# Kernel tuning notes

Hardware: AMD Instinct MI355X
Metric: run time of the kernel (lower is better)

## Reference

```python
import jax, jax.numpy as jnp
import numpy as np

D, NH, DH, DHR, DC = 2048, 16, 128, 64, 1024
B, L = 2, 2048
EPS = 1e-6


def _rms(x, w):
    return x * jax.lax.rsqrt(jnp.mean(x * x, axis=-1, keepdims=True) + EPS) * w


def _rope_tables(seq_len, dim, dtype):
    inv_freq = 1.0 / (10000.0 ** (jnp.arange(0, dim, 2, dtype=jnp.float32) / dim))
    freqs = jnp.arange(seq_len, dtype=jnp.float32)[:, None] * inv_freq[None, :]  # [L, dim/2]
    emb = jnp.concatenate([freqs, freqs], axis=-1)                               # [L, dim]
    return jnp.cos(emb).astype(dtype), jnp.sin(emb).astype(dtype)


def _apply_rope(x, cos, sin):
    # x: [B, H, L, dhr]
    half = x.shape[-1] // 2
    x1, x2 = x[..., :half], x[..., half:]
    rot = jnp.concatenate([-x2, x1], axis=-1)
    return x * cos[None, None] + rot * sin[None, None]


def setup_inputs() -> dict:
    key = jax.random.key(0)
    ks = jax.random.split(key, 14)
    s = 0.02
    inp = {
        "x": jax.random.normal(ks[0], (B, L, D), dtype=jnp.float32),
        "W_DKV": jax.random.normal(ks[1], (D, DC), dtype=jnp.float32) * s,
        "kv_norm_w": 1.0 + 0.01 * jax.random.normal(ks[2], (DC,), dtype=jnp.float32),
        "W_UK": jax.random.normal(ks[3], (DC, NH * DH), dtype=jnp.float32) * s,
        "W_UV": jax.random.normal(ks[4], (DC, NH * DH), dtype=jnp.float32) * s,
        "W_DQ": jax.random.normal(ks[5], (D, DC), dtype=jnp.float32) * s,
        "q_norm_w": 1.0 + 0.01 * jax.random.normal(ks[6], (DC,), dtype=jnp.float32),
        "W_UQ": jax.random.normal(ks[7], (DC, 2 * NH * DH), dtype=jnp.float32) * s,
        "W_QR": jax.random.normal(ks[8], (DC, 2 * NH * DHR), dtype=jnp.float32) * s,
        "W_KR": jax.random.normal(ks[9], (D, DHR), dtype=jnp.float32) * s,
        "W_lambda_w": jax.random.normal(ks[10], (D, NH), dtype=jnp.float32) * s,
        "W_lambda_b": jax.random.normal(ks[11], (NH,), dtype=jnp.float32) * s,
        "W_out": jax.random.normal(ks[12], (D, D), dtype=jnp.float32) * s,
    }
    return inp


def reference(x, W_DKV, kv_norm_w, W_UK, W_UV, W_DQ, q_norm_w, W_UQ, W_QR,
              W_KR, W_lambda_w, W_lambda_b, W_out):
    Bx, Lx, Dx = x.shape
    nh, dh, dhr = NH, DH, DHR
    dq = dh + dhr  # per-head query/key dim after decoupled-RoPE concat (192)
    scale = 1.0 / jnp.sqrt(jnp.asarray(dq, dtype=x.dtype))

    # MLA KV path
    c_kv = _rms(x @ W_DKV, kv_norm_w)                                   # [B,L,dc]
    k_c = (c_kv @ W_UK).reshape(Bx, Lx, nh, dh).transpose(0, 2, 1, 3)    # [B,nh,L,dh]
    v = (c_kv @ W_UV).reshape(Bx, Lx, nh, dh).transpose(0, 2, 1, 3)      # [B,nh,L,dh]

    # MLA Q path (doubled heads for Diff V2)
    c_q = _rms(x @ W_DQ, q_norm_w)                                       # [B,L,dcq]
    q_c = (c_q @ W_UQ).reshape(Bx, Lx, 2 * nh, dh).transpose(0, 2, 1, 3)  # [B,2nh,L,dh]

    # Decoupled RoPE
    cos, sin = _rope_tables(Lx, dhr, x.dtype)
    q_r = _apply_rope((c_q @ W_QR).reshape(Bx, Lx, 2 * nh, dhr).transpose(0, 2, 1, 3), cos, sin)
    k_r = _apply_rope((x @ W_KR).reshape(Bx, Lx, 1, dhr).transpose(0, 2, 1, 3), cos, sin)  # [B,1,L,dhr]

    q = jnp.concatenate([q_c, q_r], axis=-1)                             # [B,2nh,L,dq]
    k = jnp.concatenate([k_c, jnp.broadcast_to(k_r, (Bx, nh, Lx, dhr))], axis=-1)  # [B,nh,L,dq]

    # repeat_interleave(2) on K/V == pairing two consecutive Q heads with one K/V head
    qp = q.reshape(Bx, nh, 2, Lx, dq)                                    # [B,nh,2,L,dq]
    scores = jnp.einsum('bnpld,bnmd->bnplm', qp, k) * scale              # [B,nh,2,L,L]
    causal = jnp.tril(jnp.ones((Lx, Lx), dtype=bool))
    scores = jnp.where(causal[None, None, None], scores, jnp.finfo(scores.dtype).min)
    p = jax.nn.softmax(scores, axis=-1)
    attn = jnp.einsum('bnplm,bnmd->bnpld', p, v)                         # [B,nh,2,L,dh]

    attn1, attn2 = attn[:, :, 0], attn[:, :, 1]                          # [B,nh,L,dh]
    lam = jax.nn.sigmoid(x @ W_lambda_w + W_lambda_b)                    # [B,L,nh]
    lam = lam.transpose(0, 2, 1)[..., None]                              # [B,nh,L,1]
    out = (attn1 - lam * attn2).transpose(0, 2, 1, 3).reshape(Bx, Lx, Dx)
    return out @ W_out
```

## Files before the change

kernel.cpp:

```cpp
#include <hip/hip_runtime.h>
#include <cstddef>
#include <cstdint>


namespace {

constexpr int kDC = 1024, kDim = 2048;
constexpr float kScale = 0.07216878364870323f;
constexpr int kTA = 2128;

typedef __bf16 bf16x8 __attribute__((ext_vector_type(8)));
typedef float f32x4 __attribute__((ext_vector_type(4)));

__device__ __forceinline__ unsigned short f2bf(float f) {
  __bf16 h = (__bf16)f;
  return __builtin_bit_cast(unsigned short, h);
}
__device__ __forceinline__ float bf2f(unsigned short h) {
  union { unsigned int u; float f; } v; v.u = ((unsigned int)h) << 16;
  return v.f;
}
__device__ __forceinline__ f32x4 mfma16(bf16x8 a, bf16x8 b, f32x4 c) {
  return __builtin_amdgcn_mfma_f32_16x16x32_bf16(a, b, c, 0, 0, 0);
}
__device__ __forceinline__ void gl_lds16(const void* g, void* l) {
  __builtin_amdgcn_global_load_lds(
      (const __attribute__((address_space(1))) unsigned int*)g,
      (__attribute__((address_space(3))) unsigned int*)l, 16, 0, 0);
}
__device__ __forceinline__ void wait_lgkm0() {
  asm volatile("s_waitcnt lgkmcnt(0)" ::: "memory");
}

__global__ __launch_bounds__(256) void conv_bf16_kernel(const float* __restrict__ in,
                                                        unsigned short* __restrict__ out, int n4) {
  int e = blockIdx.x * 256 + threadIdx.x;
  if (e >= n4) return;
  float4 v = reinterpret_cast<const float4*>(in)[e];
  uint2 pk;
  pk.x = (unsigned int)f2bf(v.x) | ((unsigned int)f2bf(v.y) << 16);
  pk.y = (unsigned int)f2bf(v.z) | ((unsigned int)f2bf(v.w) << 16);
  reinterpret_cast<uint2*>(out)[e] = pk;
}

__global__ __launch_bounds__(256) void zero_bf16_kernel(unsigned short* __restrict__ out, int n8) {
  int e = blockIdx.x * 256 + threadIdx.x;
  if (e >= n8) return;
  reinterpret_cast<uint4*>(out)[e] = uint4{0, 0, 0, 0};
}

__global__ __launch_bounds__(256) void transpose_conv_kernel(const float* __restrict__ in,
                                                             unsigned short* __restrict__ out,
                                                             int K, int N) {
  __shared__ float t[32][33];
  int n0 = blockIdx.x * 32, k0 = blockIdx.y * 32;
  int tx = threadIdx.x & 31, ty = threadIdx.x >> 5;
#pragma unroll
  for (int i = 0; i < 4; i++) t[ty + i * 8][tx] = in[(size_t)(k0 + ty + i * 8) * N + n0 + tx];
  __syncthreads();
#pragma unroll
  for (int i = 0; i < 4; i++)
    out[(size_t)(n0 + ty + i * 8) * K + k0 + tx] = f2bf(t[tx][ty + i * 8]);
}

__global__ __launch_bounds__(256) void lamw_transpose_kernel(const float* __restrict__ in,
                                                             unsigned short* __restrict__ out) {
  int e = blockIdx.x * 256 + threadIdx.x;
  if (e >= 16 * 2048) return;
  int k = e & 2047, n = e >> 11;
  out[(size_t)(2112 + n) * 2048 + k] = f2bf(in[(size_t)k * 16 + n]);
}

template <int MODE>
__device__ __forceinline__ void epi_store(void* dst, void* dst2, int gr, int gc, int N, float v) {
  if (MODE == 0) {
    reinterpret_cast<float*>(dst)[(size_t)gr * N + gc] = v;
  } else if (MODE == 4) {
    if (gc < kTA) reinterpret_cast<float*>(dst)[(size_t)gr * kTA + gc] = v;
  } else if (MODE == 5) {
    int bb = gr >> 11, l = gr & 2047;
    unsigned short hv = f2bf(v);
    if (gc < 2048) {
      int h = gc >> 7, d2 = gc & 127;
      int d2s = d2 ^ ((l & 7) << 3);
      reinterpret_cast<unsigned short*>(dst)[((size_t)((bb * 16 + h) * 2048 + l)) * 192 + d2s] = hv;
    } else {
      int g2 = gc - 2048, h = g2 >> 7, d2 = g2 & 127;
      reinterpret_cast<unsigned short*>(dst2)[((size_t)((bb * 16 + h) * 128 + d2)) * 2048 + l] = hv;
    }
  } else if (MODE == 6) {
    int bb = gr >> 11, l = gr & 2047;
    if (gc < 4096) {
      int h2 = gc >> 7, d2 = gc & 127;
      reinterpret_cast<unsigned short*>(dst)[((size_t)((bb * 32 + h2) * 2048 + l)) * 192 + d2] =
          f2bf(v * kScale);
    } else {
      reinterpret_cast<unsigned short*>(dst2)[(size_t)gr * 2048 + (gc - 4096)] = f2bf(v);
    }
  }
}

template <int MODE>
__global__ __launch_bounds__(256) void gemm128_kernel(const unsigned short* __restrict__ A,
                                                      const unsigned short* __restrict__ Bt,
                                                      void* __restrict__ dst, void* __restrict__ dst2,
                                                      int M, int N, int K) {
  __shared__ unsigned short lds_a[128 * 32];
  __shared__ unsigned short lds_b[128 * 32];
  int tid = threadIdx.x, lane = tid & 63, w = tid >> 6;
  int quad = lane >> 4, l16 = lane & 15;
  int wr = w >> 1, wc = w & 1;
  int nwg = gridDim.x * gridDim.y;
  int bid = blockIdx.y * gridDim.x + blockIdx.x;
  int cpx = nwg >> 3;
  int swz = (bid & 7) * cpx + (bid >> 3);
  int bx = swz % gridDim.x, by = swz / gridDim.x;
  int mbase = by * 128, nbase = bx * 128;
  f32x4 acc[4][4] = {};
  int srow0 = tid >> 2, skoff = (tid & 3) * 8;
  const size_t a_base = (size_t)(mbase + srow0) * K + skoff;
  const size_t b_base = (size_t)(nbase + srow0) * K + skoff;
  unsigned short* lba0 = &lds_a[(size_t)(w * 64) * 8];
  unsigned short* lba1 = &lds_a[(size_t)(256 + w * 64) * 8];
  unsigned short* lbb0 = &lds_b[(size_t)(w * 64) * 8];
  unsigned short* lbb1 = &lds_b[(size_t)(256 + w * 64) * 8];
  for (int k0 = 0; k0 < K; k0 += 32) {
    __syncthreads();
    gl_lds16(&A[a_base + k0], lba0);
    gl_lds16(&A[a_base + (size_t)64 * K + k0], lba1);
    gl_lds16(&Bt[b_base + k0], lbb0);
    gl_lds16(&Bt[b_base + (size_t)64 * K + k0], lbb1);
    __syncthreads();
    bf16x8 af[4], bfr[4];
#pragma unroll
    for (int i = 0; i < 4; i++) {
      af[i] = *reinterpret_cast<const bf16x8*>(&lds_a[(wr * 64 + i * 16 + l16) * 32 + quad * 8]);
      bfr[i] = *reinterpret_cast<const bf16x8*>(&lds_b[(wc * 64 + i * 16 + l16) * 32 + quad * 8]);
    }
#pragma unroll
    for (int i = 0; i < 4; i++)
#pragma unroll
      for (int j = 0; j < 4; j++) acc[i][j] = mfma16(af[i], bfr[j], acc[i][j]);
  }
#pragma unroll
  for (int i = 0; i < 4; i++)
#pragma unroll
    for (int j = 0; j < 4; j++)
#pragma unroll
      for (int r = 0; r < 4; r++) {
        int gr = mbase + wr * 64 + i * 16 + quad * 4 + r;
        int gc = nbase + wc * 64 + j * 16 + l16;
        epi_store<MODE>(dst, dst2, gr, gc, N, acc[i][j][r]);
      }
}

__global__ __launch_bounds__(256) void rms_kernel(const float* __restrict__ in,
                                                  const float* __restrict__ w,
                                                  unsigned short* __restrict__ out, int colOff) {
  int row = blockIdx.x, tid = threadIdx.x;
  float4 v = reinterpret_cast<const float4*>(in + (size_t)row * kTA + colOff)[tid];
  float ss = v.x * v.x + v.y * v.y + v.z * v.z + v.w * v.w;
  ss += __shfl_xor(ss, 1); ss += __shfl_xor(ss, 2); ss += __shfl_xor(ss, 4);
  ss += __shfl_xor(ss, 8); ss += __shfl_xor(ss, 16); ss += __shfl_xor(ss, 32);
  __shared__ float red[4];
  if ((tid & 63) == 0) red[tid >> 6] = ss;
  __syncthreads();
  float tot = red[0] + red[1] + red[2] + red[3];
  float rs = rsqrtf(tot * (1.0f / kDC) + 1e-6f);
  float4 wv = reinterpret_cast<const float4*>(w)[tid];
  uint2 pk;
  pk.x = (unsigned int)f2bf(v.x * rs * wv.x) | ((unsigned int)f2bf(v.y * rs * wv.y) << 16);
  pk.y = (unsigned int)f2bf(v.z * rs * wv.z) | ((unsigned int)f2bf(v.w * rs * wv.w) << 16);
  reinterpret_cast<uint2*>(out)[(size_t)row * 256 + tid] = pk;
}

__device__ __forceinline__ float rope_val(float x1, float x2, int j, int l) {
  int i = j & 31;
  float inv_freq = powf(10000.0f, -(float)i * (1.0f / 32.0f));
  float ang = (float)l * inv_freq;
  float cv = cosf(ang), sv = sinf(ang);
  float rot = (j < 32) ? -x2 : x2;
  return x1 * cv + rot * sv;
}

__global__ __launch_bounds__(256) void rope_q_kernel(const unsigned short* __restrict__ qr_raw,
                                                     unsigned short* __restrict__ q_all) {
  size_t e = (size_t)blockIdx.x * 256 + threadIdx.x;
  int j = (int)(e & 63);
  int h2 = (int)((e >> 6) & 31);
  int bl = (int)(e >> 11);
  int l = bl & 2047, b = bl >> 11;
  float x1 = bf2f(qr_raw[(size_t)bl * 2048 + h2 * 64 + j]);
  float x2 = bf2f(qr_raw[(size_t)bl * 2048 + h2 * 64 + (j ^ 32)]);
  float val = rope_val(x1, x2, j, l) * kScale;
  q_all[((size_t)((b * 32 + h2) * 2048 + l)) * 192 + 128 + j] = f2bf(val);
}

__global__ __launch_bounds__(256) void rope_k_kernel(const float* __restrict__ tmpAll,
                                                     unsigned short* __restrict__ k_all) {
  size_t e = (size_t)blockIdx.x * 256 + threadIdx.x;
  int j = (int)(e & 63);
  int bl = (int)(e >> 6);
  int l = bl & 2047, b = bl >> 11;
  float x1 = tmpAll[(size_t)bl * kTA + 2048 + j];
  float x2 = tmpAll[(size_t)bl * kTA + 2048 + (j ^ 32)];
  unsigned short hv = f2bf(rope_val(x1, x2, j, l));
  int js = j ^ ((l & 7) << 3);
#pragma unroll
  for (int h = 0; h < 16; h++)
    k_all[((size_t)((b * 16 + h) * 2048 + l)) * 192 + 128 + js] = hv;
}

__global__ __launch_bounds__(256) void lam_fin_kernel(const float* __restrict__ tmpAll,
                                                      const float* __restrict__ bl_,
                                                      float* __restrict__ lam) {
  int e = blockIdx.x * 256 + threadIdx.x;
  if (e >= 4096 * 16) return;
  int n = e & 15, row = e >> 4;
  float z = tmpAll[(size_t)row * kTA + 2112 + n] + bl_[n];
  lam[e] = 1.f / (1.f + __expf(-z));
}

__global__ __launch_bounds__(256, 2) void attn7_kernel(const unsigned short* __restrict__ q_all,
                                                       const unsigned short* __restrict__ k_all,
                                                       const unsigned short* __restrict__ v_allT,
                                                       unsigned short* __restrict__ attn_o) {
  __shared__ unsigned short lds_k[2][32 * 192];
  __shared__ unsigned short lds_p[8 * 640];
  int n = blockIdx.x, qp = blockIdx.y, b = blockIdx.z;
  int tid = threadIdx.x, lane = tid & 63, w = tid >> 6, quad = lane >> 4, l16 = lane & 15;
  const unsigned short* k_head = k_all + ((size_t)(b * 16 + n) * 2048) * 192;
  const unsigned short* v_head = v_allT + ((size_t)(b * 16 + n) * 128) * 2048;

  unsigned short* pw0 = &lds_p[(w * 2 + 0) * 640];
  unsigned short* pw1 = &lds_p[(w * 2 + 1) * 640];
  const unsigned short* v_lane = v_head + (size_t)l16 * 2048 + quad * 8;

  __bf16 onec = __builtin_bit_cast(__bf16, (unsigned short)(l16 == 0 ? 0x3F80 : 0));
  bf16x8 vone = {onec, onec, onec, onec, onec, onec, onec, onec};

  auto stageK = [&](int pos0, int buf) {
    const unsigned short* kg = k_head + (size_t)pos0 * 192 + w * 1536 + lane * 8;
    unsigned short* kl = &lds_k[buf][w * 1536];
    gl_lds16(kg, kl);
    gl_lds16(kg + 512, kl + 512);
    gl_lds16(kg + 1024, kl + 1024);
  };

#pragma unroll 1
  for (int phase = 0; phase < 2; ++phase) {
    int qt = phase ? qp : (31 - qp);
    const unsigned short* q0_row =
        q_all + ((size_t)(b * 32 + 2 * n) * 2048 + qt * 64 + w * 16 + l16) * 192;
    const unsigned short* q1_row = q0_row + (size_t)2048 * 192;

    bf16x8 qf0[6], qf1[6];
#pragma unroll
    for (int ks = 0; ks < 6; ks++) {
      qf0[ks] = *reinterpret_cast<const bf16x8*>(&q0_row[ks * 32 + quad * 8]);
      qf1[ks] = *reinterpret_cast<const bf16x8*>(&q1_row[ks * 32 + quad * 8]);
    }

    f32x4 acc0[9] = {}, acc1[9] = {};
    int qlo = qt * 64 + w * 16;
    int nt = 2 * qt + 2;

    stageK(0, 0);
    for (int kt = 0; kt < nt; kt++) {
      int cur = kt & 1;
      int pos0 = kt * 32;
      __syncthreads();
      bool active = (pos0 <= qlo + 15);
      bf16x8 vf[8];
      if (active) {
        const unsigned short* vg = v_lane + pos0;
#pragma unroll
        for (int dt = 0; dt < 8; dt++)
          vf[dt] = *reinterpret_cast<const bf16x8*>(&vg[(size_t)dt * 16 * 2048]);
      }
      __builtin_amdgcn_sched_barrier(0);
      if (kt + 1 < nt) stageK((kt + 1) * 32, cur ^ 1);
      if (active) {
        const unsigned short* kb = &lds_k[cur][0];
        bool needmask = (pos0 + 31 > qlo);
        int ksw = (l16 & 7) << 3;
#pragma unroll
        for (int j = 0; j < 2; j++) {
          f32x4 s0 = {}, s1 = {};
#pragma unroll
          for (int ks = 0; ks < 6; ks++) {
            bf16x8 bK = *reinterpret_cast<const bf16x8*>(
                &kb[(j * 16 + l16) * 192 + ((ks * 32 + quad * 8) ^ ksw)]);
            s0 = mfma16(qf0[ks], bK, s0);
            s1 = mfma16(qf1[ks], bK, s1);
          }
#pragma unroll
          for (int r = 0; r < 4; r++) {
            bool msk = needmask && (pos0 + j * 16 + l16 > qlo + quad * 4 + r);
            float p0 = msk ? 0.f : __expf(s0[r]);
            float p1 = msk ? 0.f : __expf(s1[r]);
            pw0[(quad * 4 + r) * 40 + j * 16 + l16] = f2bf(p0);
            pw1[(quad * 4 + r) * 40 + j * 16 + l16] = f2bf(p1);
          }
        }
        wait_lgkm0();
        bf16x8 pf0 = *reinterpret_cast<const bf16x8*>(&pw0[l16 * 40 + quad * 8]);
        bf16x8 pf1 = *reinterpret_cast<const bf16x8*>(&pw1[l16 * 40 + quad * 8]);
#pragma unroll
        for (int dt = 0; dt < 8; dt++) {
          acc0[dt] = mfma16(pf0, vf[dt], acc0[dt]);
          acc1[dt] = mfma16(pf1, vf[dt], acc1[dt]);
        }
        acc0[8] = mfma16(pf0, vone, acc0[8]);
        acc1[8] = mfma16(pf1, vone, acc1[8]);
      }
    }

    unsigned short* o0 = attn_o + ((size_t)(b * 32 + 2 * n) * 2048 + qt * 64 + w * 16) * 128;
    unsigned short* o1 = o0 + (size_t)2048 * 128;
#pragma unroll
    for (int r = 0; r < 4; r++) {
      float li0 = __shfl(acc0[8][r], lane & 48);
      float li1 = __shfl(acc1[8][r], lane & 48);
      float inv0 = 1.f / li0, inv1 = 1.f / li1;
      int row = quad * 4 + r;
#pragma unroll
      for (int dt = 0; dt < 8; dt++) {
        o0[(size_t)row * 128 + dt * 16 + l16] = f2bf(acc0[dt][r] * inv0);
        o1[(size_t)row * 128 + dt * 16 + l16] = f2bf(acc1[dt][r] * inv1);
      }
    }
  }
}

__global__ __launch_bounds__(256) void combine_kernel(const unsigned short* __restrict__ attn_o,
                                                      const float* __restrict__ lam,
                                                      unsigned short* __restrict__ out) {
  size_t e = (size_t)blockIdx.x * 256 + threadIdx.x;
  int c8 = (int)(e & 255);
  int bl = (int)(e >> 8);
  int n = c8 >> 4, dd = (c8 & 15) * 8;
  int b = bl >> 11, l = bl & 2047;
  size_t base = ((size_t)((b * 32 + n * 2) * 2048 + l)) * 128 + dd;
  uint4 a1 = *reinterpret_cast<const uint4*>(attn_o + base);
  uint4 a2 = *reinterpret_cast<const uint4*>(attn_o + base + (size_t)2048 * 128);
  float lm = lam[(size_t)bl * 16 + n];
  unsigned int r[4];
  const unsigned int* p1 = &a1.x;
  const unsigned int* p2 = &a2.x;
#pragma unroll
  for (int i = 0; i < 4; i++) {
    float lo = bf2f((unsigned short)(p1[i] & 0xFFFF)) - lm * bf2f((unsigned short)(p2[i] & 0xFFFF));
    float hi = bf2f((unsigned short)(p1[i] >> 16)) - lm * bf2f((unsigned short)(p2[i] >> 16));
    r[i] = (unsigned int)f2bf(lo) | ((unsigned int)f2bf(hi) << 16);
  }
  *reinterpret_cast<uint4*>(out + e * 8) = uint4{r[0], r[1], r[2], r[3]};
}

}

extern "C" void kernel_launch(void* const* d_in, const int* in_sizes, int n_in,
                              void* d_out, int out_size, void* d_ws, size_t ws_size,
                              hipStream_t stream) {
  const float* x      = (const float*)d_in[0];
  const float* W_DKV  = (const float*)d_in[1];
  const float* kvnw   = (const float*)d_in[2];
  const float* W_UK   = (const float*)d_in[3];
  const float* W_UV   = (const float*)d_in[4];
  const float* W_DQ   = (const float*)d_in[5];
  const float* qnw    = (const float*)d_in[6];
  const float* W_UQ   = (const float*)d_in[7];
  const float* W_QR   = (const float*)d_in[8];
  const float* W_KR   = (const float*)d_in[9];
  const float* W_lw   = (const float*)d_in[10];
  const float* W_lb   = (const float*)d_in[11];
  const float* W_out  = (const float*)d_in[12];
  float* out = (float*)d_out;

  char* ws = (char*)d_ws;
  size_t off = 0;
  auto alloc = [&](size_t bytes) { char* p = ws + off; off += (bytes + 255) & ~(size_t)255; return p; };
  unsigned short* xb     = (unsigned short*)alloc((size_t)4096 * 2048 * 2);
  unsigned short* wd_cat = (unsigned short*)alloc((size_t)2176 * 2048 * 2);
  unsigned short* wu_cat = (unsigned short*)alloc((size_t)4096 * 1024 * 2);
  unsigned short* wuqr   = (unsigned short*)alloc((size_t)6144 * 1024 * 2);
  unsigned short* wout   = (unsigned short*)alloc((size_t)2048 * 2048 * 2);
  unsigned short* ckv    = (unsigned short*)alloc((size_t)4096 * 1024 * 2);
  unsigned short* cq     = (unsigned short*)alloc((size_t)4096 * 1024 * 2);
  unsigned short* k_all  = (unsigned short*)alloc((size_t)2 * 16 * 2048 * 192 * 2);
  unsigned short* v_allT = (unsigned short*)alloc((size_t)2 * 16 * 128 * 2048 * 2);
  unsigned short* q_all  = (unsigned short*)alloc((size_t)2 * 32 * 2048 * 192 * 2);
  unsigned short* attn_o = (unsigned short*)alloc((size_t)2 * 32 * 2048 * 128 * 2);
  unsigned short* attn_b = (unsigned short*)alloc((size_t)4096 * 2048 * 2);
  float* lam             = (float*)alloc((size_t)4096 * 16 * 4);
  float* tmpAll          = (float*)alloc((size_t)4096 * kTA * 4);
  unsigned short* tmpB   = (unsigned short*)tmpAll;
  (void)ws_size; (void)in_sizes; (void)n_in; (void)out_size;

  hipLaunchKernelGGL(conv_bf16_kernel, dim3(8192), dim3(256), 0, stream, x, xb, 2097152);
  hipLaunchKernelGGL(transpose_conv_kernel, dim3(32, 64), dim3(256), 0, stream, W_DKV, wd_cat, 2048, 1024);
  hipLaunchKernelGGL(transpose_conv_kernel, dim3(32, 64), dim3(256), 0, stream, W_DQ,
                     wd_cat + (size_t)1024 * 2048, 2048, 1024);
  hipLaunchKernelGGL(transpose_conv_kernel, dim3(2, 64), dim3(256), 0, stream, W_KR,
                     wd_cat + (size_t)2048 * 2048, 2048, 64);
  hipLaunchKernelGGL(lamw_transpose_kernel, dim3(128), dim3(256), 0, stream, W_lw, wd_cat);
  hipLaunchKernelGGL(zero_bf16_kernel, dim3(48), dim3(256), 0, stream,
                     wd_cat + (size_t)2128 * 2048, 12288);
  hipLaunchKernelGGL(transpose_conv_kernel, dim3(64, 32), dim3(256), 0, stream, W_UK, wu_cat, 1024, 2048);
  hipLaunchKernelGGL(transpose_conv_kernel, dim3(64, 32), dim3(256), 0, stream, W_UV,
                     wu_cat + (size_t)2048 * 1024, 1024, 2048);
  hipLaunchKernelGGL(transpose_conv_kernel, dim3(128, 32), dim3(256), 0, stream, W_UQ, wuqr, 1024, 4096);
  hipLaunchKernelGGL(transpose_conv_kernel, dim3(64, 32), dim3(256), 0, stream, W_QR,
                     wuqr + (size_t)4096 * 1024, 1024, 2048);
  hipLaunchKernelGGL(transpose_conv_kernel, dim3(64, 64), dim3(256), 0, stream, W_out, wout, 2048, 2048);

  hipLaunchKernelGGL(gemm128_kernel<4>, dim3(17, 32), dim3(256), 0, stream,
                     xb, wd_cat, tmpAll, (void*)nullptr, 4096, 2176, 2048);
  hipLaunchKernelGGL(rms_kernel, dim3(4096), dim3(256), 0, stream, tmpAll, kvnw, ckv, 0);
  hipLaunchKernelGGL(rms_kernel, dim3(4096), dim3(256), 0, stream, tmpAll, qnw, cq, 1024);
  hipLaunchKernelGGL(rope_k_kernel, dim3(1024), dim3(256), 0, stream, tmpAll, k_all);
  hipLaunchKernelGGL(lam_fin_kernel, dim3(256), dim3(256), 0, stream, tmpAll, W_lb, lam);

  hipLaunchKernelGGL(gemm128_kernel<5>, dim3(32, 32), dim3(256), 0, stream,
                     ckv, wu_cat, k_all, v_allT, 4096, 4096, 1024);
  hipLaunchKernelGGL(gemm128_kernel<6>, dim3(48, 32), dim3(256), 0, stream,
                     cq, wuqr, q_all, tmpB, 4096, 6144, 1024);
  hipLaunchKernelGGL(rope_q_kernel, dim3(32768), dim3(256), 0, stream, tmpB, q_all);

  hipLaunchKernelGGL(attn7_kernel, dim3(16, 16, 2), dim3(256), 0, stream,
                     q_all, k_all, v_allT, attn_o);

  hipLaunchKernelGGL(combine_kernel, dim3(4096), dim3(256), 0, stream, attn_o, lam, attn_b);
  hipLaunchKernelGGL(gemm128_kernel<0>, dim3(16, 32), dim3(256), 0, stream,
                     attn_b, wout, out, (void*)nullptr, 4096, 2048, 2048);
}
```

Before: 676.9 us.

## Double-buffer LDS tiles in GEMM kernel and use exp2f for rope frequencies

The 128x128 GEMM kernel now keeps two LDS buffers per operand. It issues the global-to-LDS loads for the next K slice before computing the MFMAs on the current slice, which removes one barrier per iteration and overlaps memory latency with compute. This doubles the LDS footprint, which may lower occupancy. The rope frequency calculation also replaces powf with an equivalent exp2f, a cheaper instruction.

```diff
diff --git a/kernel.cpp b/kernel.cpp
--- a/kernel.cpp
+++ b/kernel.cpp
@@ -105,8 +105,8 @@
                                                       const unsigned short* __restrict__ Bt,
                                                       void* __restrict__ dst, void* __restrict__ dst2,
                                                       int M, int N, int K) {
-  __shared__ unsigned short lds_a[128 * 32];
-  __shared__ unsigned short lds_b[128 * 32];
+  __shared__ unsigned short lds_a[2][128 * 32];
+  __shared__ unsigned short lds_b[2][128 * 32];
   int tid = threadIdx.x, lane = tid & 63, w = tid >> 6;
   int quad = lane >> 4, l16 = lane & 15;
   int wr = w >> 1, wc = w & 1;
@@ -120,27 +120,35 @@
   int srow0 = tid >> 2, skoff = (tid & 3) * 8;
   const size_t a_base = (size_t)(mbase + srow0) * K + skoff;
   const size_t b_base = (size_t)(nbase + srow0) * K + skoff;
-  unsigned short* lba0 = &lds_a[(size_t)(w * 64) * 8];
-  unsigned short* lba1 = &lds_a[(size_t)(256 + w * 64) * 8];
-  unsigned short* lbb0 = &lds_b[(size_t)(w * 64) * 8];
-  unsigned short* lbb1 = &lds_b[(size_t)(256 + w * 64) * 8];
-  for (int k0 = 0; k0 < K; k0 += 32) {
+  const int lofs = w * 512;
+
+  auto stageAB = [&](int k0, int buf) {
+    unsigned short* la = &lds_a[buf][lofs];
+    unsigned short* lb = &lds_b[buf][lofs];
+    gl_lds16(&A[a_base + k0], la);
+    gl_lds16(&A[a_base + (size_t)64 * K + k0], la + 2048);
+    gl_lds16(&Bt[b_base + k0], lb);
+    gl_lds16(&Bt[b_base + (size_t)64 * K + k0], lb + 2048);
+  };
+
+  stageAB(0, 0);
+  __syncthreads();
+  int nk = K >> 5;
+#pragma unroll 1
+  for (int t = 0; t < nk; ++t) {
+    int cur = t & 1;
+    if (t + 1 < nk) stageAB((t + 1) << 5, cur ^ 1);
+    bf16x8 af[4], bfr[4];
+#pragma unroll
+    for (int i = 0; i < 4; i++) {
+      af[i] = *reinterpret_cast<const bf16x8*>(&lds_a[cur][(wr * 64 + i * 16 + l16) * 32 + quad * 8]);
+      bfr[i] = *reinterpret_cast<const bf16x8*>(&lds_b[cur][(wc * 64 + i * 16 + l16) * 32 + quad * 8]);
+    }
+#pragma unroll
+    for (int i = 0; i < 4; i++)
+#pragma unroll
+      for (int j = 0; j < 4; j++) acc[i][j] = mfma16(af[i], bfr[j], acc[i][j]);
     __syncthreads();
-    gl_lds16(&A[a_base + k0], lba0);
-    gl_lds16(&A[a_base + (size_t)64 * K + k0], lba1);
-    gl_lds16(&Bt[b_base + k0], lbb0);
-    gl_lds16(&Bt[b_base + (size_t)64 * K + k0], lbb1);
-    __syncthreads();
-    bf16x8 af[4], bfr[4];
-#pragma unroll
-    for (int i = 0; i < 4; i++) {
-      af[i] = *reinterpret_cast<const bf16x8*>(&lds_a[(wr * 64 + i * 16 + l16) * 32 + quad * 8]);
-      bfr[i] = *reinterpret_cast<const bf16x8*>(&lds_b[(wc * 64 + i * 16 + l16) * 32 + quad * 8]);
-    }
-#pragma unroll
-    for (int i = 0; i < 4; i++)
-#pragma unroll
-      for (int j = 0; j < 4; j++) acc[i][j] = mfma16(af[i], bfr[j], acc[i][j]);
   }
 #pragma unroll
   for (int i = 0; i < 4; i++)
@@ -176,7 +184,7 @@
 
 __device__ __forceinline__ float rope_val(float x1, float x2, int j, int l) {
   int i = j & 31;
-  float inv_freq = powf(10000.0f, -(float)i * (1.0f / 32.0f));
+  float inv_freq = exp2f((float)i * -0.4152410119f);
   float ang = (float)l * inv_freq;
   float cv = cosf(ang), sv = sinf(ang);
   float rot = (j < 32) ? -x2 : x2;
```

New measurement: 610.7 us. -9.8%, faster.
